# Kernel optimization log

Hardware: AMD Instinct MI355X
Metric: run time of the kernel (lower is better)

## Reference

```python
import jax, jax.numpy as jnp
import numpy as np

B, S, D = 2, 2048, 2048
H, KVH = 32, 8
HD = D // H            # 64
G = H // KVH           # 4 query heads per kv head
CLIP = 8.0
THETA = 500000.0
EPS = 1e-6
SCALE = 1.0 / np.sqrt(HD)


def setup_inputs() -> dict:
    key = jax.random.key(0)
    ks = jax.random.split(key, 4)
    hidden_states = jax.random.normal(ks[0], (B, S, D), dtype=jnp.float32)
    attention_mask = jnp.ones((B, S), dtype=jnp.int32)
    position_ids = jnp.broadcast_to(jnp.arange(S, dtype=jnp.int32)[None, :], (B, S))
    causal_mask = jnp.tril(jnp.ones((S, S), dtype=bool))[None, None]
    std = 0.02
    w_qkv = jax.random.normal(ks[1], (D, D + 2 * KVH * HD), dtype=jnp.float32) * std
    w_out = jax.random.normal(ks[2], (D, D), dtype=jnp.float32) * std
    ln1_scale = jnp.ones((D,), dtype=jnp.float32)
    ln2_scale = jnp.ones((D,), dtype=jnp.float32)
    return {
        "hidden_states": hidden_states,
        "attention_mask": attention_mask,
        "position_ids": position_ids,
        "causal_mask": causal_mask,
        "ln1_scale": ln1_scale,
        "w_qkv": w_qkv,
        "w_out": w_out,
        "ln2_scale": ln2_scale,
    }


def _layernorm(x, scale):
    m = jnp.mean(x, axis=-1, keepdims=True)
    v = jnp.mean(jnp.square(x - m), axis=-1, keepdims=True)
    return (x - m) * jax.lax.rsqrt(v + EPS) * scale


def _rope(x, cos, sin):
    # neox style: rotate halves of head_dim. x: [B,S,h,HD], cos/sin: [B,S,1,HD/2]
    x1, x2 = jnp.split(x, 2, axis=-1)
    return jnp.concatenate([x1 * cos - x2 * sin, x2 * cos + x1 * sin], axis=-1)


def _forward(hidden_states, attention_mask, position_ids, causal_mask,
             ln1_scale, w_qkv, w_out, ln2_scale):
    residual = hidden_states
    x = _layernorm(hidden_states, ln1_scale)

    qkv = jnp.clip(x @ w_qkv, -CLIP, CLIP)  # [B,S,D+2*KVH*HD]
    q, kv = jnp.split(qkv, [D], axis=2)
    k, v = jnp.split(kv, [KVH * HD], axis=2)
    q = q.reshape(B, S, H, HD)
    k = k.reshape(B, S, KVH, HD)
    v = v.reshape(B, S, KVH, HD)

    inv_freq = 1.0 / (THETA ** (jnp.arange(0, HD, 2, dtype=jnp.float32) / HD))
    ang = position_ids.astype(jnp.float32)[..., None] * inv_freq  # [B,S,HD/2]
    cos = jnp.cos(ang)[:, :, None, :]
    sin = jnp.sin(ang)[:, :, None, :]
    q = _rope(q, cos, sin)
    k = _rope(k, cos, sin)

    # GQA: group query heads per kv head
    qg = q.reshape(B, S, KVH, G, HD)
    scores = jnp.einsum("bqhgd,bkhd->bhgqk", qg, k) * SCALE  # [B,KVH,G,S,S]
    mask = causal_mask[:, :, :S, :S] & (attention_mask[:, None, None, :] > 0)  # [B,1,S,S]
    bias = jnp.where(mask[:, :, None], 0.0, jnp.finfo(scores.dtype).min)
    probs = jax.nn.softmax(scores + bias, axis=-1)
    attn = jnp.einsum("bhgqk,bkhd->bqhgd", probs, v).reshape(B, S, D)

    attn_out = attn @ w_out
    hidden = attn_out + residual
    residual2 = hidden
    hidden = _layernorm(hidden, ln2_scale)
    return residual2, hidden


def reference(hidden_states, attention_mask, position_ids, causal_mask,
              ln1_scale, w_qkv, w_out, ln2_scale):
    return _forward(hidden_states, attention_mask, position_ids, causal_mask,
                    ln1_scale, w_qkv, w_out, ln2_scale)
```

## Files before the change

kernel.cpp:

```cpp
#include <hip/hip_runtime.h>
#include <hip/hip_bf16.h>
#include <stdint.h>

typedef __bf16 bf16_t;
typedef __bf16 bf16x8 __attribute__((ext_vector_type(8)));
typedef float f32x4 __attribute__((ext_vector_type(4)));
typedef _Float16 f16x8v __attribute__((ext_vector_type(8)));
typedef _Float16 f16x4v __attribute__((ext_vector_type(4)));

#define LOG2E 1.44269504088896f

__device__ __forceinline__ void load_lds16(const void* g, void* l) {
  __builtin_amdgcn_global_load_lds(
      (__attribute__((address_space(1))) unsigned int*)(uintptr_t)(g),
      (__attribute__((address_space(3))) unsigned int*)(l),
      16, 0, 0);
}

__global__ __launch_bounds__(256) void ln_kernel(
    const float* __restrict__ in, const float* __restrict__ gamma,
    bf16_t* __restrict__ out_bf, float* __restrict__ out_f)
{
  const int row = blockIdx.x;
  const int t = threadIdx.x;
  const float* x = in + (size_t)row * 2048;
  float4 a = ((const float4*)x)[t];
  float4 b = ((const float4*)x)[t + 256];
  float v[8] = {a.x, a.y, a.z, a.w, b.x, b.y, b.z, b.w};
  float s = 0.f, q = 0.f;
#pragma unroll
  for (int i = 0; i < 8; ++i) { s += v[i]; q += v[i] * v[i]; }
#pragma unroll
  for (int off = 1; off < 64; off <<= 1) {
    s += __shfl_xor(s, off, 64);
    q += __shfl_xor(q, off, 64);
  }
  __shared__ float red[4][2];
  if ((t & 63) == 0) { red[t >> 6][0] = s; red[t >> 6][1] = q; }
  __syncthreads();
  s = red[0][0] + red[1][0] + red[2][0] + red[3][0];
  q = red[0][1] + red[1][1] + red[2][1] + red[3][1];
  const float mean = s * (1.0f / 2048.0f);
  const float var = q * (1.0f / 2048.0f) - mean * mean;
  const float inv = rsqrtf(var + 1e-6f);
  float4 ga = ((const float4*)gamma)[t];
  float4 gb = ((const float4*)gamma)[t + 256];
  float g[8] = {ga.x, ga.y, ga.z, ga.w, gb.x, gb.y, gb.z, gb.w};
  float y[8];
#pragma unroll
  for (int i = 0; i < 8; ++i) y[i] = (v[i] - mean) * inv * g[i];
  if (out_bf) {
    alignas(16) bf16_t tb[8];
#pragma unroll
    for (int i = 0; i < 8; ++i) tb[i] = (bf16_t)y[i];
    bf16_t* o = out_bf + (size_t)row * 2048;
    *(uint2*)(o + t * 4) = *(const uint2*)(tb);
    *(uint2*)(o + (t + 256) * 4) = *(const uint2*)(tb + 4);
  } else {
    float* o = out_f + (size_t)row * 2048;
    ((float4*)o)[t] = make_float4(y[0], y[1], y[2], y[3]);
    ((float4*)o)[t + 256] = make_float4(y[4], y[5], y[6], y[7]);
  }
}

template <typename IT, typename OT>
__global__ __launch_bounds__(256) void transpose_cast(
    const IT* __restrict__ in, OT* __restrict__ out,
    int in_stride, int out_stride, long in_bstride, long out_bstride)
{
  const int bz = blockIdx.z;
  const IT* ib = in + (size_t)bz * in_bstride;
  OT* ob = out + (size_t)bz * out_bstride;
  const int c0 = blockIdx.x * 32, r0 = blockIdx.y * 32;
  const int tx = threadIdx.x, ty = threadIdx.y;
  __shared__ float tile[32][33];
#pragma unroll
  for (int i = 0; i < 4; ++i)
    tile[ty + i * 8][tx] = (float)ib[(size_t)(r0 + ty + i * 8) * in_stride + c0 + tx];
  __syncthreads();
#pragma unroll
  for (int i = 0; i < 4; ++i)
    ob[(size_t)(c0 + ty + i * 8) * out_stride + r0 + tx] = (OT)tile[tx][ty + i * 8];
}

__global__ __launch_bounds__(256) void gemm_bt(
    const bf16_t* __restrict__ A, const bf16_t* __restrict__ BT,
    int M, int N, int K, int mode,
    const float* __restrict__ resid, void* __restrict__ outv)
{
  __shared__ alignas(16) bf16_t As[128 * 32];
  __shared__ alignas(16) bf16_t Bs[128 * 32];
  const int t = threadIdx.x;
  const int lane = t & 63;
  const int wave = t >> 6;
  const int m0 = blockIdx.y * 128;
  const int n0 = blockIdx.x * 128;
  const int wm = (wave >> 1) * 64;
  const int wn = (wave & 1) * 64;

  f32x4 acc[4][4] = {};

  const int i0 = t, i1 = t + 256;
  const bf16_t* Ag0 = A + (size_t)(m0 + (i0 >> 2)) * K + (i0 & 3) * 8;
  const bf16_t* Ag1 = A + (size_t)(m0 + (i1 >> 2)) * K + (i1 & 3) * 8;
  const bf16_t* Bg0 = BT + (size_t)(n0 + (i0 >> 2)) * K + (i0 & 3) * 8;
  const bf16_t* Bg1 = BT + (size_t)(n0 + (i1 >> 2)) * K + (i1 & 3) * 8;
  bf16_t* AsW0 = As + (size_t)(wave * 64) * 8;
  bf16_t* AsW1 = As + (size_t)(256 + wave * 64) * 8;
  bf16_t* BsW0 = Bs + (size_t)(wave * 64) * 8;
  bf16_t* BsW1 = Bs + (size_t)(256 + wave * 64) * 8;

  const int rsel = lane & 15;
  const int ksel = (lane >> 4) * 8;

  for (int k0 = 0; k0 < K; k0 += 32) {
    __syncthreads();
    load_lds16(Ag0 + k0, AsW0);
    load_lds16(Ag1 + k0, AsW1);
    load_lds16(Bg0 + k0, BsW0);
    load_lds16(Bg1 + k0, BsW1);
    __syncthreads();
    bf16x8 af[4], bfr[4];
#pragma unroll
    for (int i = 0; i < 4; ++i) {
      af[i]  = *(const bf16x8*)(As + (wm + i * 16 + rsel) * 32 + ksel);
      bfr[i] = *(const bf16x8*)(Bs + (wn + i * 16 + rsel) * 32 + ksel);
    }
#pragma unroll
    for (int mi = 0; mi < 4; ++mi)
#pragma unroll
      for (int ni = 0; ni < 4; ++ni)
        acc[mi][ni] = __builtin_amdgcn_mfma_f32_16x16x32_bf16(af[mi], bfr[ni], acc[mi][ni], 0, 0, 0);
  }

  const int row_l = (lane >> 4) * 4;
  const int col_l = lane & 15;
#pragma unroll
  for (int mi = 0; mi < 4; ++mi) {
#pragma unroll
    for (int ni = 0; ni < 4; ++ni) {
      const size_t base = (size_t)(m0 + wm + mi * 16 + row_l) * N + (size_t)(n0 + wn + ni * 16 + col_l);
#pragma unroll
      for (int r = 0; r < 4; ++r) {
        float vv = acc[mi][ni][r];
        if (mode == 0) {
          vv = fminf(8.0f, fmaxf(-8.0f, vv));
          ((_Float16*)outv)[base + (size_t)r * N] = (_Float16)vv;
        } else {
          ((float*)outv)[base + (size_t)r * N] = vv + resid[base + (size_t)r * N];
        }
      }
    }
  }
}

__global__ __launch_bounds__(256) void rope_kernel(
    const _Float16* __restrict__ qkv, const int* __restrict__ pos_ids,
    _Float16* __restrict__ qo, _Float16* __restrict__ ko)
{
  const int bs = blockIdx.x;
  const int b = bs >> 11, s = bs & 2047;
  const float pos = (float)pos_ids[bs];
  const _Float16* row = qkv + (size_t)bs * 3072;
  const int t = threadIdx.x;
  const float qsc = 0.125f * LOG2E;
#pragma unroll
  for (int pp = 0; pp < 4; ++pp) {
    const int p = t + pp * 256;
    const int hh = p >> 5, i = p & 31;
    const float inv = exp2f(-0.59161151f * (float)i);
    float sn, cs;
    sincosf(pos * inv, &sn, &cs);
    const float x1 = (float)row[hh * 64 + i];
    const float x2 = (float)row[hh * 64 + 32 + i];
    _Float16* d = qo + (((size_t)b * 32 + hh) * 2048 + s) * 64 + i;
    d[0] = (_Float16)((x1 * cs - x2 * sn) * qsc);
    d[32] = (_Float16)((x2 * cs + x1 * sn) * qsc);
  }
  {
    const int p = t;
    const int hh = p >> 5, i = p & 31;
    const float inv = exp2f(-0.59161151f * (float)i);
    float sn, cs;
    sincosf(pos * inv, &sn, &cs);
    const float x1 = (float)row[2048 + hh * 64 + i];
    const float x2 = (float)row[2048 + hh * 64 + 32 + i];
    _Float16* d = ko + (((size_t)b * 8 + hh) * 2048 + s) * 64 + i;
    d[0] = (_Float16)(x1 * cs - x2 * sn);
    d[32] = (_Float16)(x2 * cs + x1 * sn);
  }
}

#define STAGE_TO(J, SI) do { \
    _Float16* d_ = &KV[(SI)][ksel][wv4]; \
    const _Float16* s_ = gsrc + (size_t)(J) * gstep; \
    load_lds16(s_, d_); \
    load_lds16(s_ + 32, d_ + 2048); \
  } while (0)

#define ABODY(J, BI, SI) do { \
    const int j_ = (J); \
    if (j_ == nit - 1) asm volatile("s_waitcnt vmcnt(0)" ::: "memory"); \
    else               asm volatile("s_waitcnt vmcnt(2)" ::: "memory"); \
    __builtin_amdgcn_s_barrier(); \
    __builtin_amdgcn_sched_barrier(0); \
    if (j_ + 2 < nit) STAGE_TO(j_ + 2, SI); \
    const _Float16* Kbuf = &KV[(BI)][0][0]; \
    const _Float16* Vbuf = &KV[(BI)][1][0]; \
    f32x4 st[4] = {}; \
    __builtin_amdgcn_s_setprio(1); \
    _Pragma("unroll") \
    for (int mt_ = 0; mt_ < 4; ++mt_) { \
      const f16x8v kf0_ = *(const f16x8v*)(Kbuf + krowc[mt_]); \
      const f16x8v kf1_ = *(const f16x8v*)(Kbuf + 2048 + krowc[mt_]); \
      st[mt_] = __builtin_amdgcn_mfma_f32_16x16x32_f16(kf0_, qf0, st[mt_], 0, 0, 0); \
      st[mt_] = __builtin_amdgcn_mfma_f32_16x16x32_f16(kf1_, qf1, st[mt_], 0, 0, 0); \
    } \
    __builtin_amdgcn_s_setprio(0); \
    const int k0_ = j_ * 64; \
    if (k0_ + 64 > q0) { \
      _Pragma("unroll") \
      for (int mt_ = 0; mt_ < 4; ++mt_) \
        _Pragma("unroll") \
        for (int r_ = 0; r_ < 4; ++r_) { \
          if (k0_ + mt_ * 16 + lg * 4 + r_ > myq) st[mt_][r_] = -3.0e38f; \
        } \
    } \
    float mx_ = fmaxf( \
        fmaxf(fmaxf(fmaxf(st[0][0], st[0][1]), fmaxf(st[0][2], st[0][3])), \
              fmaxf(fmaxf(st[1][0], st[1][1]), fmaxf(st[1][2], st[1][3]))), \
        fmaxf(fmaxf(fmaxf(st[2][0], st[2][1]), fmaxf(st[2][2], st[2][3])), \
              fmaxf(fmaxf(st[3][0], st[3][1]), fmaxf(st[3][2], st[3][3])))); \
    mx_ = fmaxf(mx_, __shfl_xor(mx_, 16, 64)); \
    mx_ = fmaxf(mx_, __shfl_xor(mx_, 32, 64)); \
    const bool resc_ = __any(mx_ > m_r); \
    const float mn_ = fmaxf(m_r, mx_); \
    f16x4v pf_[4]; \
    float sm_ = 0.0f; \
    _Pragma("unroll") \
    for (int mt_ = 0; mt_ < 4; ++mt_) { \
      const float p0_ = exp2f(st[mt_][0] - mn_); \
      const float p1_ = exp2f(st[mt_][1] - mn_); \
      const float p2_ = exp2f(st[mt_][2] - mn_); \
      const float p3_ = exp2f(st[mt_][3] - mn_); \
      sm_ += (p0_ + p1_) + (p2_ + p3_); \
      pf_[mt_][0] = (_Float16)p0_; pf_[mt_][1] = (_Float16)p1_; \
      pf_[mt_][2] = (_Float16)p2_; pf_[mt_][3] = (_Float16)p3_; \
    } \
    sm_ += __shfl_xor(sm_, 16, 64); \
    sm_ += __shfl_xor(sm_, 32, 64); \
    if (resc_) { \
      const float al_ = exp2f(m_r - mn_); \
      l_r = l_r * al_ + sm_; \
      _Pragma("unroll") \
      for (int r_ = 0; r_ < 4; ++r_) { \
        const float ao_ = __shfl(al_, lg * 4 + r_, 16); \
        ov[0][r_] *= ao_; ov[1][r_] *= ao_; ov[2][r_] *= ao_; ov[3][r_] *= ao_; \
      } \
    } else { \
      l_r += sm_; \
    } \
    m_r = mn_; \
    __builtin_amdgcn_s_setprio(1); \
    _Pragma("unroll") \
    for (int nt_ = 0; nt_ < 4; ++nt_) { \
      const _Float16* Vr_ = Vbuf + vrow[nt_]; \
      const f16x4v v0_ = *(const f16x4v*)(Vr_ + vca); \
      const f16x4v v1_ = *(const f16x4v*)(Vr_ + vcb); \
      const f16x4v v2_ = *(const f16x4v*)(Vr_ + 2048 + vca); \
      const f16x4v v3_ = *(const f16x4v*)(Vr_ + 2048 + vcb); \
      ov[nt_] = __builtin_amdgcn_mfma_f32_16x16x16f16(pf_[0], v0_, ov[nt_], 0, 0, 0); \
      ov[nt_] = __builtin_amdgcn_mfma_f32_16x16x16f16(pf_[1], v1_, ov[nt_], 0, 0, 0); \
      ov[nt_] = __builtin_amdgcn_mfma_f32_16x16x16f16(pf_[2], v2_, ov[nt_], 0, 0, 0); \
      ov[nt_] = __builtin_amdgcn_mfma_f32_16x16x16f16(pf_[3], v3_, ov[nt_], 0, 0, 0); \
    } \
    __builtin_amdgcn_s_setprio(0); \
  } while (0)

__global__ __launch_bounds__(512, 4) void attn_kernel(
    const _Float16* __restrict__ Q, const _Float16* __restrict__ Kb,
    const _Float16* __restrict__ Vt, bf16_t* __restrict__ Out)
{
  __shared__ alignas(16) _Float16 KV[3][2][4096];

  const int kvh = blockIdx.y;
  const int b = blockIdx.z;
  const int t = threadIdx.x;
  const int lane = t & 63;
  const int wave = t >> 6;
  const int g = wave >> 1;
  const int tile = wave & 1;
  const int h = kvh * 4 + g;
  const int ln15 = lane & 15;
  const int lg = lane >> 4;

  const _Float16* Qh = Q + ((size_t)(b * 32 + h) * 2048) * 64;
  const _Float16* Kh = Kb + ((size_t)(b * 8 + kvh) * 2048) * 64;
  const _Float16* Vh = Vt + ((size_t)(b * 8 + kvh) * 64) * 2048;

  const bool stK = (t < 256);
  const int u = t & 255;
  const int srow = u >> 2;
  const int scol = ((u & 3) ^ ((srow >> 1) & 3)) * 8;
  const _Float16* gsrc = stK ? (Kh + (size_t)srow * 64 + scol)
                             : (Vh + (size_t)srow * 2048 + scol);
  const int gstep = stK ? 64 * 64 : 64;
  const int ksel = stK ? 0 : 1;
  const int wv4 = (wave & 3) * 512;

  const int svz = (ln15 >> 1) & 3;
  const int kc = (lg ^ svz) * 8;
  const int vca = ((lg >> 1) ^ svz) * 8 + (lg & 1) * 4;
  const int vcb = (((lg >> 1) + 2) ^ svz) * 8 + (lg & 1) * 4;
  int krowc[4], vrow[4];
#pragma unroll
  for (int i = 0; i < 4; ++i) {
    krowc[i] = (i * 16 + ln15) * 32 + kc;
    vrow[i] = (i * 16 + ln15) * 32;
  }

  for (int half = 0; half < 2; ++half) {
    const int qc = (half == 0) ? blockIdx.x : (63 - blockIdx.x);
    const int q0 = qc * 32 + tile * 16;
    const int myq = q0 + ln15;
    const int nit = (qc >> 1) + 1;

    const f16x8v qf0 = *(const f16x8v*)(Qh + (size_t)(q0 + ln15) * 64 + lg * 8);
    const f16x8v qf1 = *(const f16x8v*)(Qh + (size_t)(q0 + ln15) * 64 + 32 + lg * 8);

    f32x4 ov[4] = {};
    float m_r = -3.0e38f, l_r = 0.0f;

    STAGE_TO(0, 0);
    if (nit > 1) STAGE_TO(1, 1);

    int it = 0;
    for (; it + 3 <= nit; it += 3) {
      ABODY(it, 0, 2);
      ABODY(it + 1, 1, 0);
      ABODY(it + 2, 2, 1);
    }
    if (it < nit) { ABODY(it, 0, 2); ++it; }
    if (it < nit) { ABODY(it, 1, 0); }

    const float il = 1.0f / l_r;
#pragma unroll
    for (int r = 0; r < 4; ++r) {
      const float ilo = __shfl(il, lg * 4 + r, 16);
      const size_t obase = ((size_t)b * 2048 + (size_t)(q0 + lg * 4 + r)) * 2048 + (size_t)h * 64;
#pragma unroll
      for (int nt = 0; nt < 4; ++nt)
        Out[obase + nt * 16 + ln15] = (bf16_t)(ov[nt][r] * ilo);
    }
    __builtin_amdgcn_s_barrier();
    __builtin_amdgcn_sched_barrier(0);
  }
}
#undef ABODY
#undef STAGE_TO

extern "C" void kernel_launch(void* const* d_in, const int* in_sizes, int n_in,
                              void* d_out, int out_size, void* d_ws, size_t ws_size,
                              hipStream_t stream) {
  (void)in_sizes; (void)n_in; (void)out_size; (void)ws_size;
  const float* hid  = (const float*)d_in[0];
  const int*   pos  = (const int*)d_in[2];
  const float* ln1g = (const float*)d_in[4];
  const float* wqkv = (const float*)d_in[5];
  const float* wout = (const float*)d_in[6];
  const float* ln2g = (const float*)d_in[7];
  float* out = (float*)d_out;
  char* ws = (char*)d_ws;

  bf16_t*   xb  = (bf16_t*)(ws + 0);
  bf16_t*   wT  = (bf16_t*)(ws + 16777216);
  _Float16* qkv = (_Float16*)(ws + 29360128);
  _Float16* qb  = (_Float16*)(ws + 79691776);
  _Float16* kb  = (_Float16*)(ws + 96468992);
  _Float16* vt  = (_Float16*)(ws + 100663296);

  ln_kernel<<<4096, 256, 0, stream>>>(hid, ln1g, xb, nullptr);
  transpose_cast<float, bf16_t><<<dim3(96, 64, 1), dim3(32, 8), 0, stream>>>(wqkv, wT, 3072, 2048, 0, 0);
  gemm_bt<<<dim3(24, 32), 256, 0, stream>>>(xb, wT, 4096, 3072, 2048, 0, nullptr, qkv);
  rope_kernel<<<4096, 256, 0, stream>>>(qkv, pos, qb, kb);
  transpose_cast<_Float16, _Float16><<<dim3(16, 64, 2), dim3(32, 8), 0, stream>>>(
      qkv + 2560, vt, 3072, 2048, (long)2048 * 3072, (long)512 * 2048);
  transpose_cast<float, bf16_t><<<dim3(64, 64, 1), dim3(32, 8), 0, stream>>>(wout, wT, 2048, 2048, 0, 0);
  attn_kernel<<<dim3(32, 8, 2), 512, 0, stream>>>(qb, kb, vt, xb);
  gemm_bt<<<dim3(16, 32), 256, 0, stream>>>(xb, wT, 4096, 2048, 2048, 1, hid, out);
  ln_kernel<<<4096, 256, 0, stream>>>(out, ln2g, nullptr, out + 8388608);
}
```

Baseline: 385.1 us.

## Lazy softmax rescaling, MFMA row-sum, and early V fragment loads in attention

```diff
diff --git a/kernel.cpp b/kernel.cpp
--- a/kernel.cpp
+++ b/kernel.cpp
@@ -15,6 +15,12 @@
       (__attribute__((address_space(1))) unsigned int*)(uintptr_t)(g),
       (__attribute__((address_space(3))) unsigned int*)(l),
       16, 0, 0);
+}
+
+__device__ __forceinline__ f16x4v pack4_f16(float a, float b, float c, float d) {
+  const __fp16 __attribute__((ext_vector_type(2))) lo = __builtin_amdgcn_cvt_pkrtz(a, b);
+  const __fp16 __attribute__((ext_vector_type(2))) hi = __builtin_amdgcn_cvt_pkrtz(c, d);
+  return __builtin_bit_cast(f16x4v, __builtin_shufflevector(lo, hi, 0, 1, 2, 3));
 }
 
 __global__ __launch_bounds__(256) void ln_kernel(
@@ -217,6 +223,16 @@
       st[mt_] = __builtin_amdgcn_mfma_f32_16x16x32_f16(kf1_, qf1, st[mt_], 0, 0, 0); \
     } \
     __builtin_amdgcn_s_setprio(0); \
+     \
+    f16x4v vA_[4], vB_[4], vC_[4], vD_[4]; \
+    _Pragma("unroll") \
+    for (int nt_ = 0; nt_ < 4; ++nt_) { \
+      const _Float16* Vr_ = Vbuf + vrow[nt_]; \
+      vA_[nt_] = *(const f16x4v*)(Vr_ + vca); \
+      vB_[nt_] = *(const f16x4v*)(Vr_ + vcb); \
+      vC_[nt_] = *(const f16x4v*)(Vr_ + 2048 + vca); \
+      vD_[nt_] = *(const f16x4v*)(Vr_ + 2048 + vcb); \
+    } \
     const int k0_ = j_ * 64; \
     if (k0_ + 64 > q0) { \
       _Pragma("unroll") \
@@ -226,54 +242,44 @@
           if (k0_ + mt_ * 16 + lg * 4 + r_ > myq) st[mt_][r_] = -3.0e38f; \
         } \
     } \
-    float mx_ = fmaxf( \
-        fmaxf(fmaxf(fmaxf(st[0][0], st[0][1]), fmaxf(st[0][2], st[0][3])), \
-              fmaxf(fmaxf(st[1][0], st[1][1]), fmaxf(st[1][2], st[1][3]))), \
-        fmaxf(fmaxf(fmaxf(st[2][0], st[2][1]), fmaxf(st[2][2], st[2][3])), \
-              fmaxf(fmaxf(st[3][0], st[3][1]), fmaxf(st[3][2], st[3][3])))); \
-    mx_ = fmaxf(mx_, __shfl_xor(mx_, 16, 64)); \
-    mx_ = fmaxf(mx_, __shfl_xor(mx_, 32, 64)); \
-    const bool resc_ = __any(mx_ > m_r); \
-    const float mn_ = fmaxf(m_r, mx_); \
-    f16x4v pf_[4]; \
-    float sm_ = 0.0f; \
-    _Pragma("unroll") \
-    for (int mt_ = 0; mt_ < 4; ++mt_) { \
-      const float p0_ = exp2f(st[mt_][0] - mn_); \
-      const float p1_ = exp2f(st[mt_][1] - mn_); \
-      const float p2_ = exp2f(st[mt_][2] - mn_); \
-      const float p3_ = exp2f(st[mt_][3] - mn_); \
-      sm_ += (p0_ + p1_) + (p2_ + p3_); \
-      pf_[mt_][0] = (_Float16)p0_; pf_[mt_][1] = (_Float16)p1_; \
-      pf_[mt_][2] = (_Float16)p2_; pf_[mt_][3] = (_Float16)p3_; \
-    } \
-    sm_ += __shfl_xor(sm_, 16, 64); \
-    sm_ += __shfl_xor(sm_, 32, 64); \
-    if (resc_) { \
+     \
+    const float x0_ = fmaxf(fmaxf(st[0][0], st[0][1]), st[0][2]); \
+    const float x1_ = fmaxf(fmaxf(st[0][3], st[1][0]), st[1][1]); \
+    const float x2_ = fmaxf(fmaxf(st[1][2], st[1][3]), st[2][0]); \
+    const float x3_ = fmaxf(fmaxf(st[2][1], st[2][2]), st[2][3]); \
+    const float x4_ = fmaxf(fmaxf(st[3][0], st[3][1]), st[3][2]); \
+    float mx_ = fmaxf(fmaxf(fmaxf(x0_, x1_), fmaxf(x2_, x3_)), fmaxf(x4_, st[3][3])); \
+    if (__any(mx_ > m_r + 8.0f)) {   \
+      mx_ = fmaxf(mx_, __shfl_xor(mx_, 16, 64)); \
+      mx_ = fmaxf(mx_, __shfl_xor(mx_, 32, 64)); \
+      const float mn_ = fmaxf(m_r, mx_); \
       const float al_ = exp2f(m_r - mn_); \
-      l_r = l_r * al_ + sm_; \
       _Pragma("unroll") \
       for (int r_ = 0; r_ < 4; ++r_) { \
         const float ao_ = __shfl(al_, lg * 4 + r_, 16); \
         ov[0][r_] *= ao_; ov[1][r_] *= ao_; ov[2][r_] *= ao_; ov[3][r_] *= ao_; \
+        ovl[r_] *= ao_; \
       } \
-    } else { \
-      l_r += sm_; \
-    } \
-    m_r = mn_; \
+      m_r = mn_; \
+    } \
+    f16x4v pf_[4]; \
+    _Pragma("unroll") \
+    for (int mt_ = 0; mt_ < 4; ++mt_) { \
+      pf_[mt_] = pack4_f16(exp2f(st[mt_][0] - m_r), exp2f(st[mt_][1] - m_r), \
+                           exp2f(st[mt_][2] - m_r), exp2f(st[mt_][3] - m_r)); \
+    } \
     __builtin_amdgcn_s_setprio(1); \
     _Pragma("unroll") \
     for (int nt_ = 0; nt_ < 4; ++nt_) { \
-      const _Float16* Vr_ = Vbuf + vrow[nt_]; \
-      const f16x4v v0_ = *(const f16x4v*)(Vr_ + vca); \
-      const f16x4v v1_ = *(const f16x4v*)(Vr_ + vcb); \
-      const f16x4v v2_ = *(const f16x4v*)(Vr_ + 2048 + vca); \
-      const f16x4v v3_ = *(const f16x4v*)(Vr_ + 2048 + vcb); \
-      ov[nt_] = __builtin_amdgcn_mfma_f32_16x16x16f16(pf_[0], v0_, ov[nt_], 0, 0, 0); \
-      ov[nt_] = __builtin_amdgcn_mfma_f32_16x16x16f16(pf_[1], v1_, ov[nt_], 0, 0, 0); \
-      ov[nt_] = __builtin_amdgcn_mfma_f32_16x16x16f16(pf_[2], v2_, ov[nt_], 0, 0, 0); \
-      ov[nt_] = __builtin_amdgcn_mfma_f32_16x16x16f16(pf_[3], v3_, ov[nt_], 0, 0, 0); \
-    } \
+      ov[nt_] = __builtin_amdgcn_mfma_f32_16x16x16f16(pf_[0], vA_[nt_], ov[nt_], 0, 0, 0); \
+      ov[nt_] = __builtin_amdgcn_mfma_f32_16x16x16f16(pf_[1], vB_[nt_], ov[nt_], 0, 0, 0); \
+      ov[nt_] = __builtin_amdgcn_mfma_f32_16x16x16f16(pf_[2], vC_[nt_], ov[nt_], 0, 0, 0); \
+      ov[nt_] = __builtin_amdgcn_mfma_f32_16x16x16f16(pf_[3], vD_[nt_], ov[nt_], 0, 0, 0); \
+    } \
+    ovl = __builtin_amdgcn_mfma_f32_16x16x16f16(pf_[0], onesv, ovl, 0, 0, 0); \
+    ovl = __builtin_amdgcn_mfma_f32_16x16x16f16(pf_[1], onesv, ovl, 0, 0, 0); \
+    ovl = __builtin_amdgcn_mfma_f32_16x16x16f16(pf_[2], onesv, ovl, 0, 0, 0); \
+    ovl = __builtin_amdgcn_mfma_f32_16x16x16f16(pf_[3], onesv, ovl, 0, 0, 0); \
     __builtin_amdgcn_s_setprio(0); \
   } while (0)
 
@@ -318,6 +324,7 @@
     krowc[i] = (i * 16 + ln15) * 32 + kc;
     vrow[i] = (i * 16 + ln15) * 32;
   }
+  const f16x4v onesv = {(_Float16)1.0f, (_Float16)1.0f, (_Float16)1.0f, (_Float16)1.0f};
 
   for (int half = 0; half < 2; ++half) {
     const int qc = (half == 0) ? blockIdx.x : (63 - blockIdx.x);
@@ -329,7 +336,8 @@
     const f16x8v qf1 = *(const f16x8v*)(Qh + (size_t)(q0 + ln15) * 64 + 32 + lg * 8);
 
     f32x4 ov[4] = {};
-    float m_r = -3.0e38f, l_r = 0.0f;
+    f32x4 ovl = {};
+    float m_r = 0.0f;
 
     STAGE_TO(0, 0);
     if (nit > 1) STAGE_TO(1, 1);
@@ -343,10 +351,9 @@
     if (it < nit) { ABODY(it, 0, 2); ++it; }
     if (it < nit) { ABODY(it, 1, 0); }
 
-    const float il = 1.0f / l_r;
 #pragma unroll
     for (int r = 0; r < 4; ++r) {
-      const float ilo = __shfl(il, lg * 4 + r, 16);
+      const float ilo = 1.0f / ovl[r];
       const size_t obase = ((size_t)b * 2048 + (size_t)(q0 + lg * 4 + r)) * 2048 + (size_t)h * 64;
 #pragma unroll
       for (int nt = 0; nt < 4; ++nt)
```

New measurement: 372.9 us. 3.2% less time.
